# Optimization experiments

Hardware: AMD Instinct MI355X
Metric: run time of the kernel (lower is better)

Reference implementation:

```python
import jax, jax.numpy as jnp
import numpy as np

T = 4            # number of node types (len(output_sizes))
N = 16384        # nodes per type
D_IN = 512       # input_size
D_H = 1024       # hidden_size
OUT_SIZES = (128, 96, 64, 32)
MAX_OUT = max(OUT_SIZES)


def setup_inputs() -> dict:
    key = jax.random.key(0)
    ks = jax.random.split(key, 16)
    inp = {}
    for t in range(T):
        inp[f"x{t}"] = jax.random.normal(ks[t], (N, D_IN), jnp.float32)
    # nodes are grouped by type (sorted), matching the padded dict layout
    inp["node_type"] = jnp.repeat(jnp.arange(T, dtype=jnp.int64), N)
    # layer1: per-type Linear(input_size, hidden_size) (apply_net)
    inp["W1"] = jax.random.normal(ks[4], (T, D_IN, D_H), jnp.float32) * 0.02
    inp["b1"] = jnp.zeros((T, D_H), jnp.float32)
    # layer2: per-type Linear(hidden_size, out_size_t)
    for t in range(T):
        inp[f"W2_{t}"] = jax.random.normal(ks[5 + t], (D_H, OUT_SIZES[t]), jnp.float32) * 0.02
        inp[f"b2_{t}"] = jnp.zeros((OUT_SIZES[t],), jnp.float32)
    return inp


def reference(x0, x1, x2, x3, node_type, W1, b1,
              W2_0, b2_0, W2_1, b2_1, W2_2, b2_2, W2_3, b2_3):
    # Per-type gather is implicit: x{t} already holds the features of the
    # nodes whose node_type == t (node_type is sorted/blocked).
    xs = jnp.stack([x0, x1, x2, x3])                       # [T, N, D_IN]
    # apply_net: layer1 per type + activation (batched grouped-GEMM)
    h = jax.nn.relu(jnp.einsum('tni,tih->tnh', xs, W1) + b1[:, None, :])  # [T, N, D_H]
    W2s = (W2_0, W2_1, W2_2, W2_3)
    b2s = (b2_0, b2_1, b2_2, b2_3)
    outs = []
    for t in range(T):  # fixed small set of structurally distinct heads
        o = h[t] @ W2s[t] + b2s[t]                         # [N, out_t]
        outs.append(jnp.pad(o, ((0, 0), (0, MAX_OUT - o.shape[1]))))  # _pad to MAX_OUT
    return jnp.stack(outs)                                 # [T, N, MAX_OUT]
```

## Files before the change

kernel.cpp:

```cpp
#include <hip/hip_runtime.h>
#include <hip/hip_bf16.h>


typedef __attribute__((ext_vector_type(8))) short short8;
typedef __attribute__((ext_vector_type(4))) float f32x4;

#define NT 4
#define NNODE 16384
#define DIN 512
#define DH 1024
#define MAXO 128

static __device__ __forceinline__ ushort f2bf(float f) {
    __hip_bfloat16 h = __float2bfloat16(f);
    return *reinterpret_cast<ushort*>(&h);
}

static __device__ __forceinline__ short8 pack8(const float4 a, const float4 b) {
    union { short8 v; ushort u[8]; } r;
    r.u[0] = f2bf(a.x); r.u[1] = f2bf(a.y); r.u[2] = f2bf(a.z); r.u[3] = f2bf(a.w);
    r.u[4] = f2bf(b.x); r.u[5] = f2bf(b.y); r.u[6] = f2bf(b.z); r.u[7] = f2bf(b.w);
    return r.v;
}

#define GLD(gsrc, ldst)                                                        \
    __builtin_amdgcn_global_load_lds(                                          \
        (const __attribute__((address_space(1))) void*)(gsrc),                 \
        (__attribute__((address_space(3))) void*)(ldst), 16, 0, 0)

__global__ __launch_bounds__(256) void cvt_w_t_kernel(
    const float* __restrict__ in, ushort* __restrict__ out,
    int R, int Cin, size_t in_tstride, size_t out_tstride) {
    __shared__ float tile[32][33];
    const int t = blockIdx.z;
    in += (size_t)t * in_tstride;
    out += (size_t)t * out_tstride;
    const int c0 = blockIdx.x * 32, r0 = blockIdx.y * 32;
    const int cx = threadIdx.x & 31;
    const int ry = threadIdx.x >> 5;
#pragma unroll
    for (int j = 0; j < 4; ++j) {
        int rr = ry + j * 8;
        int c = c0 + cx;
        tile[rr][cx] = (c < Cin) ? in[(size_t)(r0 + rr) * Cin + c] : 0.0f;
    }
    __syncthreads();
#pragma unroll
    for (int j = 0; j < 4; ++j) {
        int cc = ry + j * 8;
        out[(size_t)(c0 + cc) * R + r0 + cx] = f2bf(tile[cx][cc]);
    }
}

__global__ __launch_bounds__(256) void cvt_w2_kernel(
    const float* __restrict__ w0, const float* __restrict__ w1,
    const float* __restrict__ w2, const float* __restrict__ w3,
    const float* __restrict__ c0_, const float* __restrict__ c1_,
    const float* __restrict__ c2_, const float* __restrict__ c3_,
    ushort* __restrict__ out, float* __restrict__ b2p) {
    __shared__ float tile[32][33];
    const int t = blockIdx.z;
    const int Cin = (t == 0) ? 128 : (t == 1) ? 96 : (t == 2) ? 64 : 32;
    const float* in = (t == 0) ? w0 : (t == 1) ? w1 : (t == 2) ? w2 : w3;
    ushort* o = out + (size_t)t * MAXO * DH;
    const int c0 = blockIdx.x * 32, r0 = blockIdx.y * 32;
    const int cx = threadIdx.x & 31;
    const int ry = threadIdx.x >> 5;
#pragma unroll
    for (int j = 0; j < 4; ++j) {
        int rr = ry + j * 8;
        int c = c0 + cx;
        tile[rr][cx] = (c < Cin) ? in[(size_t)(r0 + rr) * Cin + c] : 0.0f;
    }
    __syncthreads();
#pragma unroll
    for (int j = 0; j < 4; ++j) {
        int cc = ry + j * 8;
        o[(size_t)(c0 + cc) * DH + r0 + cx] = f2bf(tile[cx][cc]);
    }
    if (blockIdx.x == 0 && blockIdx.y == 0 && threadIdx.x < 128) {
        const float* b = (t == 0) ? c0_ : (t == 1) ? c1_ : (t == 2) ? c2_ : c3_;
        const int n = threadIdx.x;
        b2p[t * 128 + n] = (n < Cin) ? b[n] : 0.0f;
    }
}

__global__ __launch_bounds__(512, 1) void gemm1p(
    const float* __restrict__ x0, const float* __restrict__ x1,
    const float* __restrict__ x2, const float* __restrict__ x3,
    const ushort* __restrict__ W1T, const float* __restrict__ b1,
    ushort* __restrict__ H) {
    constexpr int K = DIN;
    __shared__ char lds[147456];

    const int cpx = gridDim.x >> 3;
    const int g = blockIdx.x;
    const int wg = (g & 7) * cpx + (g >> 3);
    const int t = wg >> 8;
    const int m0 = (wg & 255) * 64;

    const float* Af = (t == 0) ? x0 : (t == 1) ? x1 : (t == 2) ? x2 : x3;
    const ushort* Bt = W1T + (size_t)t * DH * K;
    const float* bias = b1 + (size_t)t * DH;
    ushort* Ht = H + (size_t)t * NNODE * DH;

    const int tid = threadIdx.x;
    const int lane = tid & 63;
    const int w = tid >> 6;
    const int lrow = lane & 15, lgrp = lane >> 4;

    const int ar_ = tid >> 3, ac8 = tid & 7;
    const float* asrc = Af + (size_t)(m0 + ar_) * K + ac8 * 8;
    const int adst = ar_ * 128 + ((ac8 * 16) ^ ((ar_ & 7) << 4));

    const ushort* bsrc[8];
    int bdst[8];
#pragma unroll
    for (int j = 0; j < 8; ++j) {
        const int c = j * 512 + tid;
        const int r = c >> 3;
        const int cb = ((c & 7) * 16) ^ ((r & 7) << 4);
        bsrc[j] = Bt + (size_t)r * K + (cb >> 1);
        bdst[j] = c * 16;
    }

    f32x4 acc[4][8] = {};
    float4 fa0, fa1;

    fa0 = *reinterpret_cast<const float4*>(asrc);
    fa1 = *reinterpret_cast<const float4*>(asrc + 4);
#pragma unroll
    for (int j = 0; j < 8; ++j) GLD(bsrc[j], lds + bdst[j]);
    asm volatile("s_waitcnt vmcnt(8)" ::: "memory");
    *reinterpret_cast<short8*>(lds + 131072 + adst) = pack8(fa0, fa1);
    asm volatile("s_waitcnt vmcnt(0) lgkmcnt(0)" ::: "memory");
    __builtin_amdgcn_s_barrier();
    asm volatile("" ::: "memory");

#pragma unroll
    for (int j = 0; j < 16; ++j) {
        const int k = j >> 1, h = j & 1;

        if (h == 0 && k + 1 < 8) {
            fa0 = *reinterpret_cast<const float4*>(asrc + (k + 1) * 64);
            fa1 = *reinterpret_cast<const float4*>(asrc + (k + 1) * 64 + 4);
        }
        if (j + 1 < 16) {
            const int k2 = (j + 1) >> 1, h2 = (j + 1) & 1;
            const size_t off = (size_t)(h2 * 512) * K + k2 * 64;
            char* nb = lds + ((j + 1) & 1) * 65536;
#pragma unroll
            for (int jj = 0; jj < 8; ++jj) GLD(bsrc[jj] + off, nb + bdst[jj]);
        }
        if (h == 1 && k + 1 < 8)
            *reinterpret_cast<short8*>(
                lds + 131072 + ((k + 1) & 1) * 8192 + adst) = pack8(fa0, fa1);

        const char* Bl = lds + (j & 1) * 65536;
        const char* Al = lds + 131072 + (k & 1) * 8192;
#pragma unroll
        for (int kkk = 0; kkk < 2; ++kkk) {
            short8 bfr[4], af[4];
#pragma unroll
            for (int ni = 0; ni < 4; ++ni) {
                const int br = ni * 128 + w * 16 + lrow;
                const int kb = (kkk * 64 + lgrp * 16) ^ ((br & 7) << 4);
                bfr[ni] = *(const short8*)(Bl + br * 128 + kb);
            }
#pragma unroll
            for (int ml = 0; ml < 4; ++ml) {
                const int ar = ml * 16 + lrow;
                const int kb = (kkk * 64 + lgrp * 16) ^ ((ar & 7) << 4);
                af[ml] = *(const short8*)(Al + ar * 128 + kb);
            }
#pragma unroll
            for (int ml = 0; ml < 4; ++ml)
#pragma unroll
                for (int ni = 0; ni < 4; ++ni)
                    acc[ml][h * 4 + ni] = __builtin_amdgcn_mfma_f32_16x16x32_bf16(
                        bfr[ni], af[ml], acc[ml][h * 4 + ni], 0, 0, 0);
        }

        if (j + 1 < 16) {
            asm volatile("s_waitcnt vmcnt(0) lgkmcnt(0)" ::: "memory");
            __builtin_amdgcn_s_barrier();
            asm volatile("" ::: "memory");
        }
    }

#pragma unroll
    for (int niG = 0; niG < 8; ++niG) {
        const int ncol = niG * 128 + w * 16 + lgrp * 4;
        const float4 bv = *reinterpret_cast<const float4*>(&bias[ncol]);
#pragma unroll
        for (int ml = 0; ml < 4; ++ml) {
            const int row = m0 + ml * 16 + lrow;
            float v0 = fmaxf(acc[ml][niG][0] + bv.x, 0.0f);
            float v1 = fmaxf(acc[ml][niG][1] + bv.y, 0.0f);
            float v2 = fmaxf(acc[ml][niG][2] + bv.z, 0.0f);
            float v3 = fmaxf(acc[ml][niG][3] + bv.w, 0.0f);
            uint2 p;
            p.x = (uint)f2bf(v0) | ((uint)f2bf(v1) << 16);
            p.y = (uint)f2bf(v2) | ((uint)f2bf(v3) << 16);
            *reinterpret_cast<uint2*>(&Ht[(size_t)row * DH + ncol]) = p;
        }
    }
}

__global__ __launch_bounds__(512, 1) void gemm2k(
    const ushort* __restrict__ Hbase, const ushort* __restrict__ Bbase,
    const float* __restrict__ biasbase, float* __restrict__ Cbase,
    int N, int K, int MT) {
    constexpr int NF = 2;
    constexpr int NBC = 2;
    constexpr int ABYTES = 256 * 64 * 2;
    constexpr int BBYTES = 128 * 64 * 2;
    constexpr int BUF = ABYTES + BBYTES;
    __shared__ char lds[2 * BUF];

    const int cpx = gridDim.x >> 3;
    const int g = blockIdx.x;
    const int wg = (g & 7) * cpx + (g >> 3);
    const int t = wg / MT;
    const int m0 = (wg % MT) * 256;

    const ushort* A = Hbase + (size_t)t * NNODE * DH;
    const ushort* Bp = Bbase + (size_t)t * MAXO * DH;
    const float* bias = biasbase + (size_t)t * MAXO;

    const int tid = threadIdx.x;
    const int lane = tid & 63;
    const int w = tid >> 6;
    const int wm = w >> 2, wn = w & 3;
    const int lrow = lane & 15, lgrp = lane >> 4;

    const ushort* abfsrc[4];
    int adst[4];
#pragma unroll
    for (int j = 0; j < 4; ++j) {
        const int c = j * 512 + tid;
        const int r = c >> 3;
        const int cb = ((c & 7) * 16) ^ ((r & 7) << 4);
        abfsrc[j] = A + (size_t)(m0 + r) * K + (cb >> 1);
        adst[j] = c * 16;
    }
    const ushort* bsrc[NBC];
    int bdst[NBC];
#pragma unroll
    for (int j = 0; j < NBC; ++j) {
        const int c = j * 512 + tid;
        const int r = c >> 3;
        const int cb = ((c & 7) * 16) ^ ((r & 7) << 4);
        bsrc[j] = Bp + (size_t)r * K + (cb >> 1);
        bdst[j] = ABYTES + c * 16;
    }

    f32x4 acc[8][NF] = {};
    const int NK = K / 64;

#pragma unroll
    for (int j = 0; j < 4; ++j) GLD(abfsrc[j], lds + adst[j]);
#pragma unroll
    for (int j = 0; j < NBC; ++j) GLD(bsrc[j], lds + bdst[j]);
    asm volatile("s_waitcnt vmcnt(0)" ::: "memory");
    __builtin_amdgcn_s_barrier();
    asm volatile("" ::: "memory");

    for (int i = 0; i < NK; ++i) {
        const char* cu_ = lds + (i & 1) * BUF;
        char* nx_ = lds + ((i + 1) & 1) * BUF;
        const int ktn = (i + 1) * 64;
        const bool st = (i + 1 < NK);

        if (st) {
#pragma unroll
            for (int j = 0; j < 4; ++j) GLD(abfsrc[j] + ktn, nx_ + adst[j]);
#pragma unroll
            for (int j = 0; j < NBC; ++j) GLD(bsrc[j] + ktn, nx_ + bdst[j]);
        }

#pragma unroll
        for (int kkk = 0; kkk < 2; ++kkk) {
            short8 bfr[NF], af[8];
#pragma unroll
            for (int ni = 0; ni < NF; ++ni) {
                const int br = wn * (NF * 16) + ni * 16 + lrow;
                const int kb = (kkk * 64 + lgrp * 16) ^ ((br & 7) << 4);
                bfr[ni] = *(const short8*)(cu_ + ABYTES + br * 128 + kb);
            }
#pragma unroll
            for (int ml = 0; ml < 8; ++ml) {
                const int ar = wm * 128 + ml * 16 + lrow;
                const int kb = (kkk * 64 + lgrp * 16) ^ ((ar & 7) << 4);
                af[ml] = *(const short8*)(cu_ + ar * 128 + kb);
            }
#pragma unroll
            for (int ml = 0; ml < 8; ++ml)
#pragma unroll
                for (int ni = 0; ni < NF; ++ni)
                    acc[ml][ni] = __builtin_amdgcn_mfma_f32_16x16x32_bf16(
                        bfr[ni], af[ml], acc[ml][ni], 0, 0, 0);
        }

        if (st) {
            asm volatile("s_waitcnt vmcnt(0)" ::: "memory");
            __builtin_amdgcn_s_barrier();
            asm volatile("" ::: "memory");
        }
    }

    const int wnoff = wn * (NF * 16);
    const int wmoff = m0 + wm * 128;
#pragma unroll
    for (int ni = 0; ni < NF; ++ni) {
        const int ncol = wnoff + ni * 16 + lgrp * 4;
        const float4 bv = *reinterpret_cast<const float4*>(&bias[ncol]);
#pragma unroll
        for (int mi = 0; mi < 8; ++mi) {
            const int row = wmoff + mi * 16 + lrow;
            float4 p;
            p.x = acc[mi][ni][0] + bv.x;
            p.y = acc[mi][ni][1] + bv.y;
            p.z = acc[mi][ni][2] + bv.z;
            p.w = acc[mi][ni][3] + bv.w;
            *reinterpret_cast<float4*>(
                &Cbase[(size_t)t * NNODE * MAXO + (size_t)row * N + ncol]) = p;
        }
    }
}

extern "C" void kernel_launch(void* const* d_in, const int* in_sizes, int n_in,
                              void* d_out, int out_size, void* d_ws, size_t ws_size,
                              hipStream_t stream) {
    const float* x0 = (const float*)d_in[0];
    const float* x1 = (const float*)d_in[1];
    const float* x2 = (const float*)d_in[2];
    const float* x3 = (const float*)d_in[3];
    const float* W1 = (const float*)d_in[5];
    const float* b1 = (const float*)d_in[6];
    const float* W2[4] = {(const float*)d_in[7], (const float*)d_in[9],
                          (const float*)d_in[11], (const float*)d_in[13]};
    const float* b2[4] = {(const float*)d_in[8], (const float*)d_in[10],
                          (const float*)d_in[12], (const float*)d_in[14]};

    char* ws = (char*)d_ws;
    ushort* H   = (ushort*)ws;
    ushort* W1T = (ushort*)(ws + 134217728ull);
    ushort* W2T = (ushort*)(ws + 134217728ull + 4194304ull);
    float*  b2p = (float*)(ws + 134217728ull + 4194304ull + 1048576ull);

    cvt_w_t_kernel<<<dim3(32, 16, 4), 256, 0, stream>>>(
        W1, W1T, DIN, DH, (size_t)DIN * DH, (size_t)DH * DIN);
    cvt_w2_kernel<<<dim3(4, 32, 4), 256, 0, stream>>>(
        W2[0], W2[1], W2[2], W2[3], b2[0], b2[1], b2[2], b2[3], W2T, b2p);

    gemm1p<<<1024, 512, 0, stream>>>(x0, x1, x2, x3, W1T, b1, H);

    gemm2k<<<256, 512, 0, stream>>>(H, W2T, b2p, (float*)d_out,
                                    MAXO, DH, NNODE / 256);
}
```

Baseline: 163.6 us.

## Retile GEMM1 into small-LDS 128x128 blocks and single-buffer GEMM2 for occupancy

```diff
diff --git a/kernel.cpp b/kernel.cpp
--- a/kernel.cpp
+++ b/kernel.cpp
@@ -85,120 +85,121 @@
     }
 }
 
-__global__ __launch_bounds__(512, 1) void gemm1p(
+__global__ __launch_bounds__(256) void gemm1q(
     const float* __restrict__ x0, const float* __restrict__ x1,
     const float* __restrict__ x2, const float* __restrict__ x3,
     const ushort* __restrict__ W1T, const float* __restrict__ b1,
     ushort* __restrict__ H) {
     constexpr int K = DIN;
-    __shared__ char lds[147456];
+    __shared__ char lds[32768];
 
     const int cpx = gridDim.x >> 3;
     const int g = blockIdx.x;
     const int wg = (g & 7) * cpx + (g >> 3);
-    const int t = wg >> 8;
-    const int m0 = (wg & 255) * 64;
+    const int t = wg >> 10;
+    const int rmn = wg & 1023;
+    const int m0 = (rmn >> 3) * 128;
+    const int n0 = (rmn & 7) * 128;
 
     const float* Af = (t == 0) ? x0 : (t == 1) ? x1 : (t == 2) ? x2 : x3;
-    const ushort* Bt = W1T + (size_t)t * DH * K;
+    const ushort* Bp = W1T + (size_t)t * DH * K;
     const float* bias = b1 + (size_t)t * DH;
     ushort* Ht = H + (size_t)t * NNODE * DH;
 
     const int tid = threadIdx.x;
     const int lane = tid & 63;
     const int w = tid >> 6;
+    const int wm = w >> 1, wn = w & 1;
     const int lrow = lane & 15, lgrp = lane >> 4;
 
-    const int ar_ = tid >> 3, ac8 = tid & 7;
-    const float* asrc = Af + (size_t)(m0 + ar_) * K + ac8 * 8;
-    const int adst = ar_ * 128 + ((ac8 * 16) ^ ((ar_ & 7) << 4));
-
-    const ushort* bsrc[8];
-    int bdst[8];
-#pragma unroll
-    for (int j = 0; j < 8; ++j) {
-        const int c = j * 512 + tid;
+    const float* af32src[4];
+    const ushort* bsrc[4];
+    int adst[4], bdst[4];
+#pragma unroll
+    for (int j = 0; j < 4; ++j) {
+        const int c = j * 256 + tid;
         const int r = c >> 3;
-        const int cb = ((c & 7) * 16) ^ ((r & 7) << 4);
-        bsrc[j] = Bt + (size_t)r * K + (cb >> 1);
-        bdst[j] = c * 16;
-    }
-
-    f32x4 acc[4][8] = {};
-    float4 fa0, fa1;
-
-    fa0 = *reinterpret_cast<const float4*>(asrc);
-    fa1 = *reinterpret_cast<const float4*>(asrc + 4);
-#pragma unroll
-    for (int j = 0; j < 8; ++j) GLD(bsrc[j], lds + bdst[j]);
-    asm volatile("s_waitcnt vmcnt(8)" ::: "memory");
-    *reinterpret_cast<short8*>(lds + 131072 + adst) = pack8(fa0, fa1);
-    asm volatile("s_waitcnt vmcnt(0) lgkmcnt(0)" ::: "memory");
-    __builtin_amdgcn_s_barrier();
-    asm volatile("" ::: "memory");
-
-#pragma unroll
-    for (int j = 0; j < 16; ++j) {
-        const int k = j >> 1, h = j & 1;
-
-        if (h == 0 && k + 1 < 8) {
-            fa0 = *reinterpret_cast<const float4*>(asrc + (k + 1) * 64);
-            fa1 = *reinterpret_cast<const float4*>(asrc + (k + 1) * 64 + 4);
-        }
-        if (j + 1 < 16) {
-            const int k2 = (j + 1) >> 1, h2 = (j + 1) & 1;
-            const size_t off = (size_t)(h2 * 512) * K + k2 * 64;
-            char* nb = lds + ((j + 1) & 1) * 65536;
-#pragma unroll
-            for (int jj = 0; jj < 8; ++jj) GLD(bsrc[jj] + off, nb + bdst[jj]);
-        }
-        if (h == 1 && k + 1 < 8)
-            *reinterpret_cast<short8*>(
-                lds + 131072 + ((k + 1) & 1) * 8192 + adst) = pack8(fa0, fa1);
-
-        const char* Bl = lds + (j & 1) * 65536;
-        const char* Al = lds + 131072 + (k & 1) * 8192;
+        const int c8 = c & 7;
+        const int cb = (c8 * 16) ^ ((r & 7) << 4);
+        af32src[j] = Af + (size_t)(m0 + r) * K + c8 * 8;
+        adst[j] = r * 128 + cb;
+        bsrc[j] = Bp + (size_t)(n0 + r) * K + (cb >> 1);
+        bdst[j] = 16384 + c * 16;
+    }
+
+    f32x4 acc[4][4] = {};
+    float4 fa[4][2];
+
+#pragma unroll
+    for (int j = 0; j < 4; ++j) {
+        fa[j][0] = *reinterpret_cast<const float4*>(af32src[j]);
+        fa[j][1] = *reinterpret_cast<const float4*>(af32src[j] + 4);
+    }
+
+    for (int i = 0; i < K / 64; ++i) {
+        const int kt = i * 64;
+        const bool more = (i + 1 < K / 64);
+
+#pragma unroll
+        for (int j = 0; j < 4; ++j) GLD(bsrc[j] + kt, lds + bdst[j]);
+#pragma unroll
+        for (int j = 0; j < 4; ++j)
+            *reinterpret_cast<short8*>(lds + adst[j]) = pack8(fa[j][0], fa[j][1]);
+        asm volatile("" ::: "memory");
+        if (more) {
+#pragma unroll
+            for (int j = 0; j < 4; ++j) {
+                fa[j][0] = *reinterpret_cast<const float4*>(af32src[j] + kt + 64);
+                fa[j][1] = *reinterpret_cast<const float4*>(af32src[j] + kt + 68);
+            }
+            asm volatile("s_waitcnt vmcnt(8) lgkmcnt(0)" ::: "memory");
+        } else {
+            asm volatile("s_waitcnt vmcnt(0) lgkmcnt(0)" ::: "memory");
+        }
+        __builtin_amdgcn_s_barrier();
+        asm volatile("" ::: "memory");
+
 #pragma unroll
         for (int kkk = 0; kkk < 2; ++kkk) {
             short8 bfr[4], af[4];
 #pragma unroll
             for (int ni = 0; ni < 4; ++ni) {
-                const int br = ni * 128 + w * 16 + lrow;
+                const int br = wn * 64 + ni * 16 + lrow;
                 const int kb = (kkk * 64 + lgrp * 16) ^ ((br & 7) << 4);
-                bfr[ni] = *(const short8*)(Bl + br * 128 + kb);
+                bfr[ni] = *(const short8*)(lds + 16384 + br * 128 + kb);
             }
 #pragma unroll
             for (int ml = 0; ml < 4; ++ml) {
-                const int ar = ml * 16 + lrow;
+                const int ar = wm * 64 + ml * 16 + lrow;
                 const int kb = (kkk * 64 + lgrp * 16) ^ ((ar & 7) << 4);
-                af[ml] = *(const short8*)(Al + ar * 128 + kb);
+                af[ml] = *(const short8*)(lds + ar * 128 + kb);
             }
 #pragma unroll
             for (int ml = 0; ml < 4; ++ml)
 #pragma unroll
                 for (int ni = 0; ni < 4; ++ni)
-                    acc[ml][h * 4 + ni] = __builtin_amdgcn_mfma_f32_16x16x32_bf16(
-                        bfr[ni], af[ml], acc[ml][h * 4 + ni], 0, 0, 0);
-        }
-
-        if (j + 1 < 16) {
-            asm volatile("s_waitcnt vmcnt(0) lgkmcnt(0)" ::: "memory");
+                    acc[ml][ni] = __builtin_amdgcn_mfma_f32_16x16x32_bf16(
+                        bfr[ni], af[ml], acc[ml][ni], 0, 0, 0);
+        }
+
+        if (more) {
+            asm volatile("" ::: "memory");
             __builtin_amdgcn_s_barrier();
             asm volatile("" ::: "memory");
         }
     }
 
 #pragma unroll
-    for (int niG = 0; niG < 8; ++niG) {
-        const int ncol = niG * 128 + w * 16 + lgrp * 4;
+    for (int ni = 0; ni < 4; ++ni) {
+        const int ncol = n0 + wn * 64 + ni * 16 + lgrp * 4;
         const float4 bv = *reinterpret_cast<const float4*>(&bias[ncol]);
 #pragma unroll
         for (int ml = 0; ml < 4; ++ml) {
-            const int row = m0 + ml * 16 + lrow;
-            float v0 = fmaxf(acc[ml][niG][0] + bv.x, 0.0f);
-            float v1 = fmaxf(acc[ml][niG][1] + bv.y, 0.0f);
-            float v2 = fmaxf(acc[ml][niG][2] + bv.z, 0.0f);
-            float v3 = fmaxf(acc[ml][niG][3] + bv.w, 0.0f);
+            const int row = m0 + wm * 64 + ml * 16 + lrow;
+            float v0 = fmaxf(acc[ml][ni][0] + bv.x, 0.0f);
+            float v1 = fmaxf(acc[ml][ni][1] + bv.y, 0.0f);
+            float v2 = fmaxf(acc[ml][ni][2] + bv.z, 0.0f);
+            float v3 = fmaxf(acc[ml][ni][3] + bv.w, 0.0f);
             uint2 p;
             p.x = (uint)f2bf(v0) | ((uint)f2bf(v1) << 16);
             p.y = (uint)f2bf(v2) | ((uint)f2bf(v3) << 16);
@@ -207,16 +208,13 @@
     }
 }
 
-__global__ __launch_bounds__(512, 1) void gemm2k(
+__global__ __launch_bounds__(512, 1) void gemm2s(
     const ushort* __restrict__ Hbase, const ushort* __restrict__ Bbase,
     const float* __restrict__ biasbase, float* __restrict__ Cbase,
     int N, int K, int MT) {
     constexpr int NF = 2;
-    constexpr int NBC = 2;
     constexpr int ABYTES = 256 * 64 * 2;
-    constexpr int BBYTES = 128 * 64 * 2;
-    constexpr int BUF = ABYTES + BBYTES;
-    __shared__ char lds[2 * BUF];
+    __shared__ char lds[ABYTES + 128 * 64 * 2];
 
     const int cpx = gridDim.x >> 3;
     const int g = blockIdx.x;
@@ -244,10 +242,10 @@
         abfsrc[j] = A + (size_t)(m0 + r) * K + (cb >> 1);
         adst[j] = c * 16;
     }
-    const ushort* bsrc[NBC];
-    int bdst[NBC];
-#pragma unroll
-    for (int j = 0; j < NBC; ++j) {
+    const ushort* bsrc[2];
+    int bdst[2];
+#pragma unroll
+    for (int j = 0; j < 2; ++j) {
         const int c = j * 512 + tid;
         const int r = c >> 3;
         const int cb = ((c & 7) * 16) ^ ((r & 7) << 4);
@@ -258,26 +256,15 @@
     f32x4 acc[8][NF] = {};
     const int NK = K / 64;
 
-#pragma unroll
-    for (int j = 0; j < 4; ++j) GLD(abfsrc[j], lds + adst[j]);
-#pragma unroll
-    for (int j = 0; j < NBC; ++j) GLD(bsrc[j], lds + bdst[j]);
-    asm volatile("s_waitcnt vmcnt(0)" ::: "memory");
-    __builtin_amdgcn_s_barrier();
-    asm volatile("" ::: "memory");
-
     for (int i = 0; i < NK; ++i) {
-        const char* cu_ = lds + (i & 1) * BUF;
-        char* nx_ = lds + ((i + 1) & 1) * BUF;
-        const int ktn = (i + 1) * 64;
-        const bool st = (i + 1 < NK);
-
-        if (st) {
-#pragma unroll
-            for (int j = 0; j < 4; ++j) GLD(abfsrc[j] + ktn, nx_ + adst[j]);
-#pragma unroll
-            for (int j = 0; j < NBC; ++j) GLD(bsrc[j] + ktn, nx_ + bdst[j]);
-        }
+        const int kt = i * 64;
+#pragma unroll
+        for (int j = 0; j < 4; ++j) GLD(abfsrc[j] + kt, lds + adst[j]);
+#pragma unroll
+        for (int j = 0; j < 2; ++j) GLD(bsrc[j] + kt, lds + bdst[j]);
+        asm volatile("s_waitcnt vmcnt(0)" ::: "memory");
+        __builtin_amdgcn_s_barrier();
+        asm volatile("" ::: "memory");
 
 #pragma unroll
         for (int kkk = 0; kkk < 2; ++kkk) {
@@ -286,13 +273,13 @@
             for (int ni = 0; ni < NF; ++ni) {
                 const int br = wn * (NF * 16) + ni * 16 + lrow;
                 const int kb = (kkk * 64 + lgrp * 16) ^ ((br & 7) << 4);
-                bfr[ni] = *(const short8*)(cu_ + ABYTES + br * 128 + kb);
+                bfr[ni] = *(const short8*)(lds + ABYTES + br * 128 + kb);
             }
 #pragma unroll
             for (int ml = 0; ml < 8; ++ml) {
                 const int ar = wm * 128 + ml * 16 + lrow;
                 const int kb = (kkk * 64 + lgrp * 16) ^ ((ar & 7) << 4);
-                af[ml] = *(const short8*)(cu_ + ar * 128 + kb);
+                af[ml] = *(const short8*)(lds + ar * 128 + kb);
             }
 #pragma unroll
             for (int ml = 0; ml < 8; ++ml)
@@ -302,8 +289,8 @@
                         bfr[ni], af[ml], acc[ml][ni], 0, 0, 0);
         }
 
-        if (st) {
-            asm volatile("s_waitcnt vmcnt(0)" ::: "memory");
+        if (i + 1 < NK) {
+            asm volatile("" ::: "memory");
             __builtin_amdgcn_s_barrier();
             asm volatile("" ::: "memory");
         }
@@ -354,8 +341,8 @@
     cvt_w2_kernel<<<dim3(4, 32, 4), 256, 0, stream>>>(
         W2[0], W2[1], W2[2], W2[3], b2[0], b2[1], b2[2], b2[3], W2T, b2p);
 
-    gemm1p<<<1024, 512, 0, stream>>>(x0, x1, x2, x3, W1T, b1, H);
-
-    gemm2k<<<256, 512, 0, stream>>>(H, W2T, b2p, (float*)d_out,
+    gemm1q<<<4096, 256, 0, stream>>>(x0, x1, x2, x3, W1T, b1, H);
+
+    gemm2s<<<256, 512, 0, stream>>>(H, W2T, b2p, (float*)d_out,
                                     MAXO, DH, NNODE / 256);
 }
```

New measurement: 193.8 us. 18.4% more time.
